# Kernel tuning notes

Hardware: AMD Instinct MI355X
Metric: run time of the kernel (lower is better)

The kernel has to match this reference:

```python
import jax, jax.numpy as jnp
import numpy as np

N_FZ, N_KEZ, N_TINT, N_ALPHA = 60, 20, 30, 200
NORB, NTIMES = 2000, 1000


def setup_inputs() -> dict:
    key = jax.random.key(0)
    k1, k2, k3, k4 = jax.random.split(key, 4)
    # log-spaced coordinate axes (as built in __init__ from fZs / alphas)
    log_fZs = jnp.linspace(-11.0, -9.0, N_FZ, dtype=jnp.float32)
    log_alphas = jnp.linspace(-2.0, 0.0, N_ALPHA, dtype=jnp.float32)
    alphas = 10.0 ** log_alphas
    kEZs = jnp.linspace(0.5, 10.0, N_KEZ, dtype=jnp.float32)  # sorted for searchsorted
    # grid already in stored layout (n_fZ, n_kEZ, n_tint, n_alpha)
    grid = 20.0 + 5.0 * jax.random.uniform(k1, (N_FZ, N_KEZ, N_TINT, N_ALPHA), dtype=jnp.float32)
    # angular separations, mostly inside [alphas[0], alphas[-1]] with some outside
    alpha = 10.0 ** jax.random.uniform(k2, (NORB, NTIMES), minval=-2.2, maxval=0.1, dtype=jnp.float32)
    dMag = 20.0 + 5.0 * jax.random.uniform(k3, (NORB, NTIMES), dtype=jnp.float32)
    fZ_vals = 10.0 ** jax.random.uniform(k4, (NTIMES,), minval=-11.0, maxval=-9.0, dtype=jnp.float32)
    kEZ_val = jnp.asarray(3.0, dtype=jnp.float32)
    return dict(alpha=alpha, dMag=dMag, fZ_vals=fZ_vals, kEZ_val=kEZ_val,
                grid=grid, kEZs=kEZs, alphas=alphas, log_fZs=log_fZs, log_alphas=log_alphas)


def reference(alpha, dMag, fZ_vals, kEZ_val, grid, kEZs, alphas, log_fZs, log_alphas):
    """Faithful translation of dMag0Grid._pdet_alpha_dMag.

    alpha, dMag : (norb, ntimes); fZ_vals : (ntimes,); kEZ_val : scalar.
    grid : (n_fZ, n_kEZ, n_tint, n_alpha).  Returns pdet : (ntimes, n_tint).
    """
    n_fZ = grid.shape[0]
    n_alpha = grid.shape[-1]
    inv_log_fZ_step = 1.0 / (log_fZs[1] - log_fZs[0])
    inv_log_alpha_step = 1.0 / (log_alphas[1] - log_alphas[0])

    geom_mask = (alpha >= alphas[0]) & (alpha <= alphas[-1])  # (norb, ntimes)

    # log-binned fZ index, per time
    fZ_ind = (jnp.log10(fZ_vals) - log_fZs[0]) * inv_log_fZ_step
    fZ0 = jnp.clip(jnp.floor(fZ_ind).astype(jnp.int32) + 1, 0, n_fZ - 2)  # (ntimes,)

    # log-binned alpha index, per (orbit, time)
    a_ind = (jnp.log10(alpha) - log_alphas[0]) * inv_log_alpha_step
    a0 = jnp.clip(a_ind.astype(jnp.int32), 0, n_alpha - 1)  # (norb, ntimes)
    dalpha = (a_ind - a0).astype(grid.dtype)

    kEZ_ind = jnp.searchsorted(kEZs, kEZ_val, side='right') - 1  # scalar

    # dynamic_slice clamps start so the size-2 window stays in bounds
    a0s = jnp.minimum(a0, n_alpha - 2)
    fZb = jnp.broadcast_to(fZ0[None, :], a0.shape)  # (norb, ntimes)

    sub = grid[:, kEZ_ind]          # (n_fZ, n_tint, n_alpha)
    g0 = sub[fZb, :, a0s]           # (norb, ntimes, n_tint) gather
    g1 = sub[fZb, :, a0s + 1]
    dim = g0 + dalpha[..., None] * (g1 - g0)  # linear interp in log-alpha

    det_mask = geom_mask[..., None] & jnp.signbit(dMag[..., None] - dim)
    pdet = det_mask.mean(axis=0)    # (ntimes, n_tint)
    return pdet
```

## Files before the change

### kernel.cpp

```cpp
#include <hip/hip_runtime.h>
#include <math.h>

#define N_FZ    60
#define N_KEZ   20
#define N_TINT  30
#define N_ALPHA 200
#define NORB    2000
#define NTIMES  1000
#define BLOCK   256

__global__ __launch_bounds__(BLOCK) void pdet_kernel(
    const float* __restrict__ alpha,
    const float* __restrict__ dMag,
    const float* __restrict__ fZ_vals,
    const float* __restrict__ kEZ_val,
    const float* __restrict__ grid,
    const float* __restrict__ kEZs,
    const float* __restrict__ alphas,
    const float* __restrict__ log_fZs,
    const float* __restrict__ log_alphas,
    float* __restrict__ out)
{
    __shared__ float2 pairs[N_TINT * N_ALPHA];
    __shared__ int    wsum[BLOCK / 64][N_TINT];

    const int t   = blockIdx.x;
    const int tid = threadIdx.x;

    const float la0    = log_alphas[0];
    const float inv_la = 1.0f / (log_alphas[1] - la0);
    const float alo    = alphas[0];
    const float ahi    = alphas[N_ALPHA - 1];

    const float lf0    = log_fZs[0];
    const float lfstep = log_fZs[1] - lf0;
    double fZ_ind = (log10((double)fZ_vals[t]) - (double)lf0) * (1.0 / (double)lfstep);
    int fZ0 = (int)floor(fZ_ind) + 1;
    fZ0 = min(max(fZ0, 0), N_FZ - 2);

    const float kv = kEZ_val[0];
    int kidx = -1;
    #pragma unroll
    for (int i = 0; i < N_KEZ; ++i) kidx += (kEZs[i] <= kv) ? 1 : 0;
    if (kidx < 0) kidx += N_KEZ;

    const float* src = grid + ((size_t)fZ0 * N_KEZ + kidx) * (N_TINT * N_ALPHA);
    const float4* src4 = (const float4*)src;
    for (int j = tid; j < (N_TINT * N_ALPHA) / 4; j += BLOCK) {
        float4 v  = src4[j];
        float nxt = src[4 * j + 4];
        pairs[4 * j + 0] = make_float2(v.x, v.y);
        pairs[4 * j + 1] = make_float2(v.y, v.z);
        pairs[4 * j + 2] = make_float2(v.z, v.w);
        pairs[4 * j + 3] = make_float2(v.w, nxt);
    }
    __syncthreads();

    int cnt[N_TINT];
    #pragma unroll
    for (int k = 0; k < N_TINT; ++k) cnt[k] = 0;

    for (int orb = tid; orb < NORB; orb += BLOCK) {
        float a  = alpha[(size_t)orb * NTIMES + t];
        float dm = dMag [(size_t)orb * NTIMES + t];
        bool geom = (a >= alo) && (a <= ahi);
        float a_ind = (log10f(a) - la0) * inv_la;
        int a0 = (int)a_ind;
        a0 = min(max(a0, 0), N_ALPHA - 1);
        float dal = a_ind - (float)a0;
        int a0s = min(a0, N_ALPHA - 2);
        if (!geom) dm = __builtin_inff();

        #pragma unroll
        for (int k = 0; k < N_TINT; ++k) {
            float2 p = pairs[k * N_ALPHA + a0s];
            float dim = p.x + dal * (p.y - p.x);
            cnt[k] += (dm < dim) ? 1 : 0;
        }
    }

    const int lane = tid & 63;
    const int wid  = tid >> 6;
    #pragma unroll
    for (int k = 0; k < N_TINT; ++k) {
        int c = cnt[k];
        c += __shfl_xor(c, 32, 64);
        c += __shfl_xor(c, 16, 64);
        c += __shfl_xor(c,  8, 64);
        c += __shfl_xor(c,  4, 64);
        c += __shfl_xor(c,  2, 64);
        c += __shfl_xor(c,  1, 64);
        if (lane == 0) wsum[wid][k] = c;
    }
    __syncthreads();

    if (tid < N_TINT) {
        int tot = wsum[0][tid] + wsum[1][tid] + wsum[2][tid] + wsum[3][tid];
        out[(size_t)t * N_TINT + tid] = (float)tot / (float)NORB;
    }
}

extern "C" void kernel_launch(void* const* d_in, const int* in_sizes, int n_in,
                              void* d_out, int out_size, void* d_ws, size_t ws_size,
                              hipStream_t stream) {
    const float* alpha      = (const float*)d_in[0];
    const float* dMag       = (const float*)d_in[1];
    const float* fZ_vals    = (const float*)d_in[2];
    const float* kEZ_val    = (const float*)d_in[3];
    const float* grid       = (const float*)d_in[4];
    const float* kEZs       = (const float*)d_in[5];
    const float* alphas     = (const float*)d_in[6];
    const float* log_fZs    = (const float*)d_in[7];
    const float* log_alphas = (const float*)d_in[8];
    float* out = (float*)d_out;

    pdet_kernel<<<NTIMES, BLOCK, 0, stream>>>(
        alpha, dMag, fZ_vals, kEZ_val, grid, kEZs, alphas, log_fZs, log_alphas, out);
}
```

Before: 134.2 us.

## Precompute log-alpha index and masked dMag in transposed workspace layout

Adds a prep kernel that computes the log-alpha fractional index and geometry-masked dMag per (orbit, time), then writes them as float2 in a time-major layout through a shared-memory transpose. The main kernel then reads each time's row contiguously with float4 loads and processes two orbits per iteration. This replaces the strided column reads of the original kernel (stride NTIMES per orbit) and moves the log10 work out of the per-block loop. The cost is an extra launch plus a 16 MB workspace write and read, and the path only runs if the workspace is large enough.

```diff
diff --git a/kernel.cpp b/kernel.cpp
--- a/kernel.cpp
+++ b/kernel.cpp
@@ -9,17 +9,144 @@
 #define NTIMES  1000
 #define BLOCK   256
 
-__global__ __launch_bounds__(BLOCK) void pdet_kernel(
+__global__ __launch_bounds__(256) void prep_kernel(
     const float* __restrict__ alpha,
     const float* __restrict__ dMag,
+    const float* __restrict__ alphas,
+    const float* __restrict__ log_alphas,
+    float2* __restrict__ xd)
+{
+    __shared__ float2 tile[32][33];
+
+    const float la0    = log_alphas[0];
+    const float inv_la = 1.0f / (log_alphas[1] - la0);
+    const float alo    = alphas[0];
+    const float ahi    = alphas[N_ALPHA - 1];
+
+    const int t0 = blockIdx.x * 32;
+    const int o0 = blockIdx.y * 32;
+    const int tx = threadIdx.x, ty = threadIdx.y;
+
+    #pragma unroll
+    for (int r = 0; r < 4; ++r) {
+        int orb = o0 + ty + 8 * r;
+        int t   = t0 + tx;
+        float2 v = make_float2(0.0f, __builtin_inff());
+        if (orb < NORB && t < NTIMES) {
+            float a  = alpha[(size_t)orb * NTIMES + t];
+            float dm = dMag [(size_t)orb * NTIMES + t];
+            bool geom = (a >= alo) && (a <= ahi);
+            float x = (log10f(a) - la0) * inv_la;
+            v = make_float2(x, geom ? dm : __builtin_inff());
+        }
+        tile[ty + 8 * r][tx] = v;
+    }
+    __syncthreads();
+    #pragma unroll
+    for (int r = 0; r < 4; ++r) {
+        int tt  = ty + 8 * r;
+        int t   = t0 + tt;
+        int orb = o0 + tx;
+        if (orb < NORB && t < NTIMES)
+            xd[(size_t)t * NORB + orb] = tile[tx][tt];
+    }
+}
+
+__global__ __launch_bounds__(BLOCK) void pdet2_kernel(
+    const float2* __restrict__ xd,
     const float* __restrict__ fZ_vals,
     const float* __restrict__ kEZ_val,
     const float* __restrict__ grid,
     const float* __restrict__ kEZs,
-    const float* __restrict__ alphas,
     const float* __restrict__ log_fZs,
-    const float* __restrict__ log_alphas,
     float* __restrict__ out)
+{
+    __shared__ float2 pairs[N_TINT * N_ALPHA];
+    __shared__ int    wsum[BLOCK / 64][N_TINT];
+
+    const int t   = blockIdx.x;
+    const int tid = threadIdx.x;
+
+    const float lf0    = log_fZs[0];
+    const float lfstep = log_fZs[1] - lf0;
+    double fZ_ind = (log10((double)fZ_vals[t]) - (double)lf0) * (1.0 / (double)lfstep);
+    int fZ0 = (int)floor(fZ_ind) + 1;
+    fZ0 = min(max(fZ0, 0), N_FZ - 2);
+
+    const float kv = kEZ_val[0];
+    int kidx = -1;
+    #pragma unroll
+    for (int i = 0; i < N_KEZ; ++i) kidx += (kEZs[i] <= kv) ? 1 : 0;
+    if (kidx < 0) kidx += N_KEZ;
+
+    const float* src = grid + ((size_t)fZ0 * N_KEZ + kidx) * (N_TINT * N_ALPHA);
+    const float4* src4 = (const float4*)src;
+    for (int j = tid; j < (N_TINT * N_ALPHA) / 4; j += BLOCK) {
+        float4 v  = src4[j];
+        float nxt = src[4 * j + 4];
+        pairs[4 * j + 0] = make_float2(v.x, v.y);
+        pairs[4 * j + 1] = make_float2(v.y, v.z);
+        pairs[4 * j + 2] = make_float2(v.z, v.w);
+        pairs[4 * j + 3] = make_float2(v.w, nxt);
+    }
+    __syncthreads();
+
+    int cnt[N_TINT];
+    #pragma unroll
+    for (int k = 0; k < N_TINT; ++k) cnt[k] = 0;
+
+    const float4* row = (const float4*)(xd + (size_t)t * NORB);
+    for (int i = tid; i < NORB / 2; i += BLOCK) {
+        float4 v = row[i];
+        float xA = v.x, dmA = v.y;
+        float xB = v.z, dmB = v.w;
+
+        int   a0A = min(max((int)xA, 0), N_ALPHA - 1);
+        float dalA = xA - (float)a0A;
+        int   aA  = min(a0A, N_ALPHA - 2);
+
+        int   a0B = min(max((int)xB, 0), N_ALPHA - 1);
+        float dalB = xB - (float)a0B;
+        int   aB  = min(a0B, N_ALPHA - 2);
+
+        #pragma unroll
+        for (int k = 0; k < N_TINT; ++k) {
+            float2 pA = pairs[k * N_ALPHA + aA];
+            float2 pB = pairs[k * N_ALPHA + aB];
+            float dimA = pA.x + dalA * (pA.y - pA.x);
+            float dimB = pB.x + dalB * (pB.y - pB.x);
+            cnt[k] += (dmA < dimA) ? 1 : 0;
+            cnt[k] += (dmB < dimB) ? 1 : 0;
+        }
+    }
+
+    const int lane = tid & 63;
+    const int wid  = tid >> 6;
+    #pragma unroll
+    for (int k = 0; k < N_TINT; ++k) {
+        int c = cnt[k];
+        c += __shfl_xor(c, 32, 64);
+        c += __shfl_xor(c, 16, 64);
+        c += __shfl_xor(c,  8, 64);
+        c += __shfl_xor(c,  4, 64);
+        c += __shfl_xor(c,  2, 64);
+        c += __shfl_xor(c,  1, 64);
+        if (lane == 0) wsum[wid][k] = c;
+    }
+    __syncthreads();
+
+    if (tid < N_TINT) {
+        int tot = wsum[0][tid] + wsum[1][tid] + wsum[2][tid] + wsum[3][tid];
+        out[(size_t)t * N_TINT + tid] = (float)tot / (float)NORB;
+    }
+}
+
+__global__ __launch_bounds__(BLOCK) void pdet_kernel(
+    const float* __restrict__ alpha, const float* __restrict__ dMag,
+    const float* __restrict__ fZ_vals, const float* __restrict__ kEZ_val,
+    const float* __restrict__ grid, const float* __restrict__ kEZs,
+    const float* __restrict__ alphas, const float* __restrict__ log_fZs,
+    const float* __restrict__ log_alphas, float* __restrict__ out)
 {
     __shared__ float2 pairs[N_TINT * N_ALPHA];
     __shared__ int    wsum[BLOCK / 64][N_TINT];
@@ -114,6 +241,17 @@
     const float* log_alphas = (const float*)d_in[8];
     float* out = (float*)d_out;
 
-    pdet_kernel<<<NTIMES, BLOCK, 0, stream>>>(
-        alpha, dMag, fZ_vals, kEZ_val, grid, kEZs, alphas, log_fZs, log_alphas, out);
-}
+    const size_t need = (size_t)NTIMES * NORB * sizeof(float2);
+    if (ws_size >= need) {
+        dim3 gb((NTIMES + 31) / 32, (NORB + 31) / 32);
+        dim3 tb(32, 8);
+        prep_kernel<<<gb, tb, 0, stream>>>(alpha, dMag, alphas, log_alphas,
+                                           (float2*)d_ws);
+        pdet2_kernel<<<NTIMES, BLOCK, 0, stream>>>(
+            (const float2*)d_ws, fZ_vals, kEZ_val, grid, kEZs, log_fZs, out);
+    } else {
+        pdet_kernel<<<NTIMES, BLOCK, 0, stream>>>(
+            alpha, dMag, fZ_vals, kEZ_val, grid, kEZs, alphas, log_fZs,
+            log_alphas, out);
+    }
+}
```

Measured after the change: 136.5 us. Within noise of the previous version (+1.7%).
